# Optimization experiments

Measured on AMD Instinct MI355X. Metric: run time of the kernel, lower is better.

The kernel has to match this reference:

```python
import jax, jax.numpy as jnp
import numpy as np

N_NODES = 100000
N_EDGES = 1600000
NUM_FEATURES = 128
HIDDEN = 64
NUM_CLASSES = 2


def _gcn_norm(edge_index, num_nodes):
    # PyG gcn_norm: add self-loops, symmetric degree normalization.
    loop = jnp.arange(num_nodes, dtype=edge_index.dtype)
    src = jnp.concatenate([edge_index[0], loop])
    dst = jnp.concatenate([edge_index[1], loop])
    deg = jax.ops.segment_sum(jnp.ones_like(src, dtype=jnp.float32), dst,
                              num_segments=num_nodes)
    dinv = jnp.where(deg > 0, jax.lax.rsqrt(deg), 0.0)
    norm = dinv[src] * dinv[dst]  # [E + N]
    return src, dst, norm


def _gcn_conv(x, src, dst, norm, W, b, num_nodes):
    h = x @ W  # linear transform first (PyG GCNConv)
    msg = h[src] * norm[:, None]  # gather + edge scaling, [E+N, H]
    out = jax.ops.segment_sum(msg, dst, num_segments=num_nodes)  # scatter-add
    return out + b


def setup_inputs() -> dict:
    key = jax.random.key(0)
    ks = jax.random.split(key, 8)
    x = jax.random.normal(ks[0], (N_NODES, NUM_FEATURES), dtype=jnp.float32)
    edge_index = jax.random.randint(ks[1], (2, N_EDGES), 0, N_NODES, dtype=jnp.int32)
    def glorot(k, shape):
        lim = np.sqrt(6.0 / (shape[0] + shape[1]))
        return jax.random.uniform(k, shape, jnp.float32, -lim, lim)
    return {
        "x": x,
        "edge_index": edge_index,
        "W1": glorot(ks[2], (NUM_FEATURES, HIDDEN)),
        "b1": jnp.zeros((HIDDEN,), jnp.float32),
        "W2": glorot(ks[3], (HIDDEN, HIDDEN)),
        "b2": jnp.zeros((HIDDEN,), jnp.float32),
        "W3": glorot(ks[4], (HIDDEN, HIDDEN)),
        "b3": jnp.zeros((HIDDEN,), jnp.float32),
        "Wlin": glorot(ks[5], (HIDDEN, NUM_CLASSES)),
        "blin": jnp.zeros((NUM_CLASSES,), jnp.float32),
    }


def reference(x, edge_index, W1, b1, W2, b2, W3, b3, Wlin, blin):
    num_nodes = x.shape[0]
    src, dst, norm = _gcn_norm(edge_index, num_nodes)
    # eval mode: dropout is identity
    h = jax.nn.relu(_gcn_conv(x, src, dst, norm, W1, b1, num_nodes))
    h = jax.nn.relu(_gcn_conv(h, src, dst, norm, W2, b2, num_nodes))
    h = jax.nn.relu(_gcn_conv(h, src, dst, norm, W3, b3, num_nodes))
    logits = h @ Wlin + blin
    return jax.nn.log_softmax(logits, axis=1)
```

## Files before the change

kernel.cpp:

```cpp
#include <hip/hip_runtime.h>
#include <cstdint>
#include <cstddef>

#define NF 128
#define NH 64

typedef unsigned int uint32;
typedef short bf16x8 __attribute__((ext_vector_type(8)));
typedef float f32x4 __attribute__((ext_vector_type(4)));

__device__ inline unsigned short f2bf(float f) {
  unsigned int u = __float_as_uint(f);
  return (unsigned short)((u + 0x7FFF + ((u >> 16) & 1)) >> 16);
}
__device__ inline float bf2f_lo(uint32 u) { return __uint_as_float(u << 16); }
__device__ inline float bf2f_hi(uint32 u) { return __uint_as_float(u & 0xFFFF0000u); }


__global__ __launch_bounds__(256) void count_kernel(const int* __restrict__ ei, int E,
                                                    int* __restrict__ cnt, int RW) {
  int pass = blockIdx.x & 3;
  int i = (blockIdx.x >> 2) * 256 + threadIdx.x;
  if (i * 4 >= E) return;
  int4 d = ((const int4*)(ei + E))[i];
  int lo = pass * RW, hi = lo + RW;
  if (d.x >= lo && d.x < hi) atomicAdd(&cnt[d.x], 1);
  if (d.y >= lo && d.y < hi) atomicAdd(&cnt[d.y], 1);
  if (d.z >= lo && d.z < hi) atomicAdd(&cnt[d.z], 1);
  if (d.w >= lo && d.w < hi) atomicAdd(&cnt[d.w], 1);
}

__global__ __launch_bounds__(256) void partial_kernel(const int* __restrict__ cnt, int N,
                                                      int* __restrict__ part) {
  __shared__ int sd[256];
  int t = threadIdx.x;
  int idx = blockIdx.x * 1024 + t * 4;
  int s = 0;
#pragma unroll
  for (int j = 0; j < 4; ++j)
    if (idx + j < N) s += cnt[idx + j];
  sd[t] = s;
  __syncthreads();
  for (int off = 128; off > 0; off >>= 1) {
    if (t < off) sd[t] += sd[t + off];
    __syncthreads();
  }
  if (t == 0) part[blockIdx.x] = sd[0];
}

__global__ __launch_bounds__(128) void scanp_kernel(int* __restrict__ part, int NB,
                                                    int* __restrict__ rowptrN) {
  __shared__ int s[128];
  int t = threadIdx.x;
  int v = (t < NB) ? part[t] : 0;
  s[t] = v;
  __syncthreads();
  for (int off = 1; off < 128; off <<= 1) {
    int add = (t >= off) ? s[t - off] : 0;
    __syncthreads();
    s[t] += add;
    __syncthreads();
  }
  if (t < NB) part[t] = s[t] - v;
  if (t == 0) rowptrN[0] = s[127];
}

__global__ __launch_bounds__(256) void rowptr_kernel(const int* __restrict__ cnt,
                                                     const int* __restrict__ part,
                                                     int* __restrict__ rowptr,
                                                     int* __restrict__ cnt2,
                                                     float* __restrict__ dinv, int N) {
  __shared__ int s[256];
  int t = threadIdx.x;
  int idx = blockIdx.x * 1024 + t * 4;
  int c[4];
  int ts = 0;
#pragma unroll
  for (int j = 0; j < 4; ++j) {
    c[j] = (idx + j < N) ? cnt[idx + j] : 0;
    ts += c[j];
  }
  s[t] = ts;
  __syncthreads();
  for (int off = 1; off < 256; off <<= 1) {
    int add = (t >= off) ? s[t - off] : 0;
    __syncthreads();
    s[t] += add;
    __syncthreads();
  }
  int run = s[t] - ts + part[blockIdx.x];
#pragma unroll
  for (int j = 0; j < 4; ++j) {
    if (idx + j < N) {
      rowptr[idx + j] = run;
      cnt2[idx + j] = run;
      dinv[idx + j] = rsqrtf((float)(c[j] + 1));
    }
    run += c[j];
  }
}

__global__ __launch_bounds__(256) void fill_kernel(const int* __restrict__ ei, int E,
                                                   int* __restrict__ cnt2,
                                                   const float* __restrict__ dinv,
                                                   int2* __restrict__ col2, int RW) {
  int pass = blockIdx.x & 3;
  int i = (blockIdx.x >> 2) * 256 + threadIdx.x;
  if (i * 4 >= E) return;
  int4 sv = ((const int4*)ei)[i];
  int4 dv = ((const int4*)(ei + E))[i];
  int lo = pass * RW, hi = lo + RW;
  int ss[4] = {sv.x, sv.y, sv.z, sv.w};
  int dd[4] = {dv.x, dv.y, dv.z, dv.w};
#pragma unroll
  for (int j = 0; j < 4; ++j) {
    int d = dd[j];
    if (d < lo || d >= hi) continue;
    int s = ss[j];
    float w = dinv[s] * dinv[d];
    int pos = atomicAdd(&cnt2[d], 1);
    col2[pos] = make_int2(s, __float_as_int(w));
  }
}


__global__ __launch_bounds__(256) void gemm1_mfma_kernel(
    const float* __restrict__ X, const float* __restrict__ W,
    uint32* __restrict__ Hb, int N) {
  const int lane = threadIdx.x & 63;
  const int wv = threadIdx.x >> 6;
  const int m = lane & 15;
  const int g = lane >> 4;
  const int base = blockIdx.x * 64 + wv * 16;
  int row = base + m;
  int rowc = row < N ? row : N - 1;
  const float* xp = X + (size_t)rowc * 128 + g * 8;

  f32x4 acc[4];
#pragma unroll
  for (int nt = 0; nt < 4; ++nt) acc[nt] = (f32x4){0.f, 0.f, 0.f, 0.f};

#pragma unroll
  for (int kk = 0; kk < 4; ++kk) {
    float4 alo = *(const float4*)(xp + kk * 32);
    float4 ahi = *(const float4*)(xp + kk * 32 + 4);
    bf16x8 a;
    a[0] = (short)f2bf(alo.x); a[1] = (short)f2bf(alo.y);
    a[2] = (short)f2bf(alo.z); a[3] = (short)f2bf(alo.w);
    a[4] = (short)f2bf(ahi.x); a[5] = (short)f2bf(ahi.y);
    a[6] = (short)f2bf(ahi.z); a[7] = (short)f2bf(ahi.w);
    const float* wp = W + (size_t)(kk * 32 + g * 8) * 64 + m;
#pragma unroll
    for (int nt = 0; nt < 4; ++nt) {
      bf16x8 b;
#pragma unroll
      for (int i = 0; i < 8; ++i)
        b[i] = (short)f2bf(wp[(size_t)i * 64 + nt * 16]);
      acc[nt] = __builtin_amdgcn_mfma_f32_16x16x32_bf16(a, b, acc[nt], 0, 0, 0);
    }
  }
  unsigned short* Hs = (unsigned short*)Hb;
#pragma unroll
  for (int j = 0; j < 4; ++j) {
    int n = base + g * 4 + j;
    if (n < N) {
#pragma unroll
      for (int nt = 0; nt < 4; ++nt)
        Hs[(size_t)n * 64 + nt * 16 + m] = f2bf(acc[nt][j]);
    }
  }
}


template <int FINAL>
__global__ __launch_bounds__(256) void prop_fused_kernel(
    const uint32* __restrict__ H32, const int* __restrict__ rowptr,
    const int2* __restrict__ col2, const float* __restrict__ dinv,
    const float* __restrict__ bias, const float* __restrict__ Wn,
    const float* __restrict__ blin, void* __restrict__ outv, int N) {
  __shared__ float Ws[FINAL ? 4 : 64 * 64];
  __shared__ float rbuf[FINAL ? 1 : 4][64];
  const int lane = threadIdx.x & 63;
  const int widx = threadIdx.x >> 6;
  const int fl = lane & 31;
  const int half = lane >> 5;

  if (!FINAL) {
    const float4* Wg = (const float4*)Wn;
    float4* Wl = (float4*)Ws;
    for (int i = threadIdx.x; i < 1024; i += 256) Wl[i] = Wg[i];
    __syncthreads();
  }

  int n = blockIdx.x * 4 + widx;
  n = __builtin_amdgcn_readfirstlane(n);
  if (n >= N) return;

  int e0 = rowptr[n];
  int e1 = rowptr[n + 1];
  float di = dinv[n];
  const int2* ec = col2 + e0;
  const int m = e1 - e0;

  float acc0 = 0.f, acc1 = 0.f;
  if (half == 0) {
    uint32 u = H32[(size_t)n * 32 + fl];
    float w = di * di;
    acc0 = bf2f_lo(u) * w;
    acc1 = bf2f_hi(u) * w;
  }

  const int npair = m >> 1;
  const int nfull = npair >> 3;
  for (int b = 0; b < nfull; ++b) {
    int s[8];
    float wv[8];
#pragma unroll
    for (int j = 0; j < 8; ++j) {
      int2 c = ec[2 * (b * 8 + j) + half];
      s[j] = c.x;
      wv[j] = __int_as_float(c.y);
    }
    uint32 u[8];
#pragma unroll
    for (int j = 0; j < 8; ++j) u[j] = H32[(size_t)s[j] * 32 + fl];
#pragma unroll
    for (int j = 0; j < 8; ++j) {
      acc0 = fmaf(wv[j], bf2f_lo(u[j]), acc0);
      acc1 = fmaf(wv[j], bf2f_hi(u[j]), acc1);
    }
  }
  for (int t = nfull * 8; t < npair; ++t) {
    int2 c = ec[2 * t + half];
    uint32 u = H32[(size_t)c.x * 32 + fl];
    float w = __int_as_float(c.y);
    acc0 = fmaf(w, bf2f_lo(u), acc0);
    acc1 = fmaf(w, bf2f_hi(u), acc1);
  }
  if ((m & 1) && half == 0) {
    int2 c = ec[m - 1];
    uint32 u = H32[(size_t)c.x * 32 + fl];
    float w = __int_as_float(c.y);
    acc0 = fmaf(w, bf2f_lo(u), acc0);
    acc1 = fmaf(w, bf2f_hi(u), acc1);
  }
  acc0 += __shfl_xor(acc0, 32, 64);
  acc1 += __shfl_xor(acc1, 32, 64);

  float2 bv = ((const float2*)bias)[fl];
  float r0 = acc0 + bv.x;
  float r1 = acc1 + bv.y;
  r0 = r0 > 0.f ? r0 : 0.f;
  r1 = r1 > 0.f ? r1 : 0.f;

  if (FINAL) {
    float t0 = 0.f, t1 = 0.f;
    if (half == 0) {
      t0 = r0 * Wn[4 * fl + 0] + r1 * Wn[4 * fl + 2];
      t1 = r0 * Wn[4 * fl + 1] + r1 * Wn[4 * fl + 3];
    }
#pragma unroll
    for (int off = 32; off > 0; off >>= 1) {
      t0 += __shfl_xor(t0, off, 64);
      t1 += __shfl_xor(t1, off, 64);
    }
    if (lane == 0) {
      float* out = (float*)outv;
      float l0 = t0 + blin[0];
      float l1 = t1 + blin[1];
      float mx = fmaxf(l0, l1);
      float lz = mx + logf(expf(l0 - mx) + expf(l1 - mx));
      out[(size_t)n * 2 + 0] = l0 - lz;
      out[(size_t)n * 2 + 1] = l1 - lz;
    }
  } else {
    if (half == 0) *(float2*)(&rbuf[widx][2 * fl]) = make_float2(r0, r1);
    __builtin_amdgcn_wave_barrier();
    float o = 0.f;
#pragma unroll
    for (int q = 0; q < 16; ++q) {
      float4 rv = *(const float4*)(&rbuf[widx][4 * q]);
      o = fmaf(rv.x, Ws[(4 * q + 0) * 64 + lane], o);
      o = fmaf(rv.y, Ws[(4 * q + 1) * 64 + lane], o);
      o = fmaf(rv.z, Ws[(4 * q + 2) * 64 + lane], o);
      o = fmaf(rv.w, Ws[(4 * q + 3) * 64 + lane], o);
    }
    ((unsigned short*)outv)[(size_t)n * 64 + lane] = f2bf(o);
  }
}


extern "C" void kernel_launch(void* const* d_in, const int* in_sizes, int n_in,
                              void* d_out, int out_size, void* d_ws, size_t ws_size,
                              hipStream_t stream) {
  const float* x  = (const float*)d_in[0];
  const int*   ei = (const int*)d_in[1];
  const float* W1 = (const float*)d_in[2];
  const float* b1 = (const float*)d_in[3];
  const float* W2 = (const float*)d_in[4];
  const float* b2 = (const float*)d_in[5];
  const float* W3 = (const float*)d_in[6];
  const float* b3 = (const float*)d_in[7];
  const float* Wl = (const float*)d_in[8];
  const float* bl = (const float*)d_in[9];
  float* out = (float*)d_out;

  const int N = in_sizes[0] / NF;
  const int E = in_sizes[1] / 2;

  char* w = (char*)d_ws;
  size_t off = 0;
  auto alloc = [&](size_t bytes) {
    void* p = w + off;
    off += bytes;
    off = (off + 15) & ~(size_t)15;
    return p;
  };
  int*    cnt    = (int*)alloc((size_t)N * 4);
  int*    cnt2   = (int*)alloc((size_t)N * 4);
  int*    rowptr = (int*)alloc((size_t)(N + 1) * 4);
  int*    part   = (int*)alloc(256 * 4);
  float*  dinv   = (float*)alloc((size_t)N * 4);
  int2*   col2   = (int2*)alloc((size_t)E * 8);
  uint32* hA     = (uint32*)alloc((size_t)N * 32 * 4);
  uint32* hB     = (uint32*)alloc((size_t)N * 32 * 4);

  const int NB = (N + 1023) / 1024;
  const int RW4 = (N + 3) / 4;
  const int NCHUNK = (E / 4 + 255) / 256;

  hipMemsetAsync(cnt, 0, (size_t)N * 4, stream);
  hipLaunchKernelGGL(count_kernel, dim3(4 * NCHUNK), dim3(256), 0, stream,
                     ei, E, cnt, RW4);
  hipLaunchKernelGGL(partial_kernel, dim3(NB), dim3(256), 0, stream, cnt, N, part);
  hipLaunchKernelGGL(scanp_kernel, dim3(1), dim3(128), 0, stream, part, NB, rowptr + N);
  hipLaunchKernelGGL(rowptr_kernel, dim3(NB), dim3(256), 0, stream,
                     cnt, part, rowptr, cnt2, dinv, N);
  hipLaunchKernelGGL(fill_kernel, dim3(4 * NCHUNK), dim3(256), 0, stream,
                     ei, E, cnt2, dinv, col2, RW4);

  hipLaunchKernelGGL(gemm1_mfma_kernel, dim3((N + 63) / 64), dim3(256), 0, stream,
                     x, W1, hA, N);
  hipLaunchKernelGGL(prop_fused_kernel<0>, dim3((N + 3) / 4), dim3(256), 0, stream,
                     hA, rowptr, col2, dinv, b1, W2, (const float*)nullptr, (void*)hB, N);
  hipLaunchKernelGGL(prop_fused_kernel<0>, dim3((N + 3) / 4), dim3(256), 0, stream,
                     hB, rowptr, col2, dinv, b2, W3, (const float*)nullptr, (void*)hA, N);
  hipLaunchKernelGGL(prop_fused_kernel<1>, dim3((N + 3) / 4), dim3(256), 0, stream,
                     hA, rowptr, col2, dinv, b3, Wl, bl, (void*)out, N);
}
```

Measured before the change: 428.7 us.

## Fuse gemm1 with degree count; split layer-2 into sliced aggregation plus separate transform

Merges the first-layer MFMA GEMM and the edge degree-count into one launch, so the compute-bound GEMM blocks run alongside the atomic-bound counting blocks and one launch is removed. The second layer's fused aggregate-and-transform kernel is replaced by an aggregation kernel that splits the 64 features into two 32-wide slices across separate blocks, four edges per wave iteration, followed by a standalone tiled FP32 transform kernel. This aims to raise memory-level parallelism in the gather and move the dense transform out of the latency-bound gather kernel. In exchange it adds an extra bf16 write and read of the intermediate activations and reads the edge list twice.

After: 467.9 us. 9.1% more time.

```diff
diff --git a/kernel.cpp b/kernel.cpp
--- a/kernel.cpp
+++ b/kernel.cpp
@@ -17,17 +17,66 @@
 __device__ inline float bf2f_hi(uint32 u) { return __uint_as_float(u & 0xFFFF0000u); }
 
 
-__global__ __launch_bounds__(256) void count_kernel(const int* __restrict__ ei, int E,
-                                                    int* __restrict__ cnt, int RW) {
-  int pass = blockIdx.x & 3;
-  int i = (blockIdx.x >> 2) * 256 + threadIdx.x;
-  if (i * 4 >= E) return;
-  int4 d = ((const int4*)(ei + E))[i];
-  int lo = pass * RW, hi = lo + RW;
-  if (d.x >= lo && d.x < hi) atomicAdd(&cnt[d.x], 1);
-  if (d.y >= lo && d.y < hi) atomicAdd(&cnt[d.y], 1);
-  if (d.z >= lo && d.z < hi) atomicAdd(&cnt[d.z], 1);
-  if (d.w >= lo && d.w < hi) atomicAdd(&cnt[d.w], 1);
+__global__ __launch_bounds__(256) void gemm1_count_kernel(
+    const float* __restrict__ X, const float* __restrict__ W,
+    uint32* __restrict__ Hb, int N,
+    const int* __restrict__ ei, int E, int* __restrict__ cnt, int RW, int G1) {
+  if ((int)blockIdx.x >= G1) {
+    int b = blockIdx.x - G1;
+    int pass = b & 3;
+    int i = (b >> 2) * 256 + threadIdx.x;
+    if (i * 4 >= E) return;
+    int4 d = ((const int4*)(ei + E))[i];
+    int lo = pass * RW, hi = lo + RW;
+    if (d.x >= lo && d.x < hi) atomicAdd(&cnt[d.x], 1);
+    if (d.y >= lo && d.y < hi) atomicAdd(&cnt[d.y], 1);
+    if (d.z >= lo && d.z < hi) atomicAdd(&cnt[d.z], 1);
+    if (d.w >= lo && d.w < hi) atomicAdd(&cnt[d.w], 1);
+    return;
+  }
+
+  const int lane = threadIdx.x & 63;
+  const int wv = threadIdx.x >> 6;
+  const int m = lane & 15;
+  const int g = lane >> 4;
+  const int base = blockIdx.x * 64 + wv * 16;
+  int row = base + m;
+  int rowc = row < N ? row : N - 1;
+  const float* xp = X + (size_t)rowc * 128 + g * 8;
+
+  f32x4 acc[4];
+#pragma unroll
+  for (int nt = 0; nt < 4; ++nt) acc[nt] = (f32x4){0.f, 0.f, 0.f, 0.f};
+
+#pragma unroll
+  for (int kk = 0; kk < 4; ++kk) {
+    float4 alo = *(const float4*)(xp + kk * 32);
+    float4 ahi = *(const float4*)(xp + kk * 32 + 4);
+    bf16x8 a;
+    a[0] = (short)f2bf(alo.x); a[1] = (short)f2bf(alo.y);
+    a[2] = (short)f2bf(alo.z); a[3] = (short)f2bf(alo.w);
+    a[4] = (short)f2bf(ahi.x); a[5] = (short)f2bf(ahi.y);
+    a[6] = (short)f2bf(ahi.z); a[7] = (short)f2bf(ahi.w);
+    const float* wp = W + (size_t)(kk * 32 + g * 8) * 64 + m;
+#pragma unroll
+    for (int nt = 0; nt < 4; ++nt) {
+      bf16x8 b;
+#pragma unroll
+      for (int i = 0; i < 8; ++i)
+        b[i] = (short)f2bf(wp[(size_t)i * 64 + nt * 16]);
+      acc[nt] = __builtin_amdgcn_mfma_f32_16x16x32_bf16(a, b, acc[nt], 0, 0, 0);
+    }
+  }
+  unsigned short* Hs = (unsigned short*)Hb;
+#pragma unroll
+  for (int j = 0; j < 4; ++j) {
+    int n = base + g * 4 + j;
+    if (n < N) {
+#pragma unroll
+      for (int nt = 0; nt < 4; ++nt)
+        Hs[(size_t)n * 64 + nt * 16 + m] = f2bf(acc[nt][j]);
+    }
+  }
 }
 
 __global__ __launch_bounds__(256) void partial_kernel(const int* __restrict__ cnt, int N,
@@ -124,54 +173,6 @@
 }
 
 
-__global__ __launch_bounds__(256) void gemm1_mfma_kernel(
-    const float* __restrict__ X, const float* __restrict__ W,
-    uint32* __restrict__ Hb, int N) {
-  const int lane = threadIdx.x & 63;
-  const int wv = threadIdx.x >> 6;
-  const int m = lane & 15;
-  const int g = lane >> 4;
-  const int base = blockIdx.x * 64 + wv * 16;
-  int row = base + m;
-  int rowc = row < N ? row : N - 1;
-  const float* xp = X + (size_t)rowc * 128 + g * 8;
-
-  f32x4 acc[4];
-#pragma unroll
-  for (int nt = 0; nt < 4; ++nt) acc[nt] = (f32x4){0.f, 0.f, 0.f, 0.f};
-
-#pragma unroll
-  for (int kk = 0; kk < 4; ++kk) {
-    float4 alo = *(const float4*)(xp + kk * 32);
-    float4 ahi = *(const float4*)(xp + kk * 32 + 4);
-    bf16x8 a;
-    a[0] = (short)f2bf(alo.x); a[1] = (short)f2bf(alo.y);
-    a[2] = (short)f2bf(alo.z); a[3] = (short)f2bf(alo.w);
-    a[4] = (short)f2bf(ahi.x); a[5] = (short)f2bf(ahi.y);
-    a[6] = (short)f2bf(ahi.z); a[7] = (short)f2bf(ahi.w);
-    const float* wp = W + (size_t)(kk * 32 + g * 8) * 64 + m;
-#pragma unroll
-    for (int nt = 0; nt < 4; ++nt) {
-      bf16x8 b;
-#pragma unroll
-      for (int i = 0; i < 8; ++i)
-        b[i] = (short)f2bf(wp[(size_t)i * 64 + nt * 16]);
-      acc[nt] = __builtin_amdgcn_mfma_f32_16x16x32_bf16(a, b, acc[nt], 0, 0, 0);
-    }
-  }
-  unsigned short* Hs = (unsigned short*)Hb;
-#pragma unroll
-  for (int j = 0; j < 4; ++j) {
-    int n = base + g * 4 + j;
-    if (n < N) {
-#pragma unroll
-      for (int nt = 0; nt < 4; ++nt)
-        Hs[(size_t)n * 64 + nt * 16 + m] = f2bf(acc[nt][j]);
-    }
-  }
-}
-
-
 template <int FINAL>
 __global__ __launch_bounds__(256) void prop_fused_kernel(
     const uint32* __restrict__ H32, const int* __restrict__ rowptr,
@@ -286,6 +287,127 @@
       o = fmaf(rv.w, Ws[(4 * q + 3) * 64 + lane], o);
     }
     ((unsigned short*)outv)[(size_t)n * 64 + lane] = f2bf(o);
+  }
+}
+
+
+__global__ __launch_bounds__(256) void agg_half_kernel(
+    const uint32* __restrict__ H32, const int* __restrict__ rowptr,
+    const int2* __restrict__ col2, const float* __restrict__ dinv,
+    const float* __restrict__ bias, uint32* __restrict__ Rout, int N, int NBH) {
+  const int slice = (int)blockIdx.x >= NBH ? 1 : 0;
+  const int nb = blockIdx.x - slice * NBH;
+  const int lane = threadIdx.x & 63;
+  const int widx = threadIdx.x >> 6;
+  const int fl = lane & 15;
+  const int qtr = lane >> 4;
+
+  int n = nb * 4 + widx;
+  n = __builtin_amdgcn_readfirstlane(n);
+  if (n >= N) return;
+
+  int e0 = rowptr[n];
+  int m = rowptr[n + 1] - e0;
+  const int2* ec = col2 + e0;
+  float di = dinv[n];
+  const uint32* Hs = H32 + slice * 16 + fl;
+
+  float acc0 = 0.f, acc1 = 0.f;
+  const int nq = (m + 3) >> 2;
+  for (int it = 0; it < nq; ++it) {
+    int er = it * 4 + qtr;
+    bool v = er < m;
+    int2 c = ec[v ? er : 0];
+    float w = v ? __int_as_float(c.y) : 0.f;
+    uint32 u = Hs[(size_t)c.x * 32];
+    acc0 = fmaf(w, bf2f_lo(u), acc0);
+    acc1 = fmaf(w, bf2f_hi(u), acc1);
+  }
+  acc0 += __shfl_xor(acc0, 16, 64);
+  acc1 += __shfl_xor(acc1, 16, 64);
+  acc0 += __shfl_xor(acc0, 32, 64);
+  acc1 += __shfl_xor(acc1, 32, 64);
+
+  uint32 su = Hs[(size_t)n * 32];
+  float d2 = di * di;
+  acc0 = fmaf(d2, bf2f_lo(su), acc0);
+  acc1 = fmaf(d2, bf2f_hi(su), acc1);
+
+  float2 bv = ((const float2*)bias)[slice * 16 + fl];
+  float r0 = fmaxf(acc0 + bv.x, 0.f);
+  float r1 = fmaxf(acc1 + bv.y, 0.f);
+  if (qtr == 0) {
+    Rout[(size_t)n * 32 + slice * 16 + fl] =
+        (uint32)f2bf(r0) | ((uint32)f2bf(r1) << 16);
+  }
+}
+
+__global__ __launch_bounds__(256, 4) void transform_kernel(
+    const uint32* __restrict__ R, const float* __restrict__ W,
+    uint32* __restrict__ Hout, int N) {
+  __shared__ float XsT[64][68];
+  __shared__ float Ws[64 * 64];
+  const int tid = threadIdx.x;
+  const int n0 = blockIdx.x * 64;
+  const int tn = (tid >> 4) * 4;
+  const int tf = (tid & 15) * 4;
+  {
+    const float4* Wg = (const float4*)W;
+    float4* Wl = (float4*)Ws;
+#pragma unroll
+    for (int j = 0; j < 4; ++j) Wl[tid + j * 256] = Wg[tid + j * 256];
+  }
+#pragma unroll
+  for (int it = 0; it < 2; ++it) {
+    int sb = it * 256 + tid;
+    int n = sb >> 3;
+    int q = sb & 7;
+    uint4 v = make_uint4(0, 0, 0, 0);
+    if (n0 + n < N) v = *(const uint4*)(R + (size_t)(n0 + n) * 32 + q * 4);
+    XsT[q * 8 + 0][n] = bf2f_lo(v.x);
+    XsT[q * 8 + 1][n] = bf2f_hi(v.x);
+    XsT[q * 8 + 2][n] = bf2f_lo(v.y);
+    XsT[q * 8 + 3][n] = bf2f_hi(v.y);
+    XsT[q * 8 + 4][n] = bf2f_lo(v.z);
+    XsT[q * 8 + 5][n] = bf2f_hi(v.z);
+    XsT[q * 8 + 6][n] = bf2f_lo(v.w);
+    XsT[q * 8 + 7][n] = bf2f_hi(v.w);
+  }
+  __syncthreads();
+  float acc[4][4];
+#pragma unroll
+  for (int i = 0; i < 4; ++i)
+#pragma unroll
+    for (int j = 0; j < 4; ++j) acc[i][j] = 0.f;
+#pragma unroll 8
+  for (int k = 0; k < 64; ++k) {
+    float4 xv = *(const float4*)(&XsT[k][tn]);
+    float4 wv = *(const float4*)(&Ws[k * 64 + tf]);
+    acc[0][0] = fmaf(xv.x, wv.x, acc[0][0]);
+    acc[0][1] = fmaf(xv.x, wv.y, acc[0][1]);
+    acc[0][2] = fmaf(xv.x, wv.z, acc[0][2]);
+    acc[0][3] = fmaf(xv.x, wv.w, acc[0][3]);
+    acc[1][0] = fmaf(xv.y, wv.x, acc[1][0]);
+    acc[1][1] = fmaf(xv.y, wv.y, acc[1][1]);
+    acc[1][2] = fmaf(xv.y, wv.z, acc[1][2]);
+    acc[1][3] = fmaf(xv.y, wv.w, acc[1][3]);
+    acc[2][0] = fmaf(xv.z, wv.x, acc[2][0]);
+    acc[2][1] = fmaf(xv.z, wv.y, acc[2][1]);
+    acc[2][2] = fmaf(xv.z, wv.z, acc[2][2]);
+    acc[2][3] = fmaf(xv.z, wv.w, acc[2][3]);
+    acc[3][0] = fmaf(xv.w, wv.x, acc[3][0]);
+    acc[3][1] = fmaf(xv.w, wv.y, acc[3][1]);
+    acc[3][2] = fmaf(xv.w, wv.z, acc[3][2]);
+    acc[3][3] = fmaf(xv.w, wv.w, acc[3][3]);
+  }
+#pragma unroll
+  for (int i = 0; i < 4; ++i) {
+    int n = n0 + tn + i;
+    if (n < N) {
+      uint32 a = (uint32)f2bf(acc[i][0]) | ((uint32)f2bf(acc[i][1]) << 16);
+      uint32 b = (uint32)f2bf(acc[i][2]) | ((uint32)f2bf(acc[i][3]) << 16);
+      *(uint2*)(Hout + (size_t)n * 32 + tf / 2) = make_uint2(a, b);
+    }
   }
 }
 
@@ -328,10 +450,12 @@
   const int NB = (N + 1023) / 1024;
   const int RW4 = (N + 3) / 4;
   const int NCHUNK = (E / 4 + 255) / 256;
+  const int G1 = ((((N + 63) / 64) + 3) / 4) * 4;
+  const int NBH = (N + 3) / 4;
 
   hipMemsetAsync(cnt, 0, (size_t)N * 4, stream);
-  hipLaunchKernelGGL(count_kernel, dim3(4 * NCHUNK), dim3(256), 0, stream,
-                     ei, E, cnt, RW4);
+  hipLaunchKernelGGL(gemm1_count_kernel, dim3(G1 + 4 * NCHUNK), dim3(256), 0, stream,
+                     x, W1, hA, N, ei, E, cnt, RW4, G1);
   hipLaunchKernelGGL(partial_kernel, dim3(NB), dim3(256), 0, stream, cnt, N, part);
   hipLaunchKernelGGL(scanp_kernel, dim3(1), dim3(128), 0, stream, part, NB, rowptr + N);
   hipLaunchKernelGGL(rowptr_kernel, dim3(NB), dim3(256), 0, stream,
@@ -339,12 +463,12 @@
   hipLaunchKernelGGL(fill_kernel, dim3(4 * NCHUNK), dim3(256), 0, stream,
                      ei, E, cnt2, dinv, col2, RW4);
 
-  hipLaunchKernelGGL(gemm1_mfma_kernel, dim3((N + 63) / 64), dim3(256), 0, stream,
-                     x, W1, hA, N);
-  hipLaunchKernelGGL(prop_fused_kernel<0>, dim3((N + 3) / 4), dim3(256), 0, stream,
+  hipLaunchKernelGGL(prop_fused_kernel<0>, dim3(NBH), dim3(256), 0, stream,
                      hA, rowptr, col2, dinv, b1, W2, (const float*)nullptr, (void*)hB, N);
-  hipLaunchKernelGGL(prop_fused_kernel<0>, dim3((N + 3) / 4), dim3(256), 0, stream,
-                     hB, rowptr, col2, dinv, b2, W3, (const float*)nullptr, (void*)hA, N);
-  hipLaunchKernelGGL(prop_fused_kernel<1>, dim3((N + 3) / 4), dim3(256), 0, stream,
-                     hA, rowptr, col2, dinv, b3, Wl, bl, (void*)out, N);
-}
+  hipLaunchKernelGGL(agg_half_kernel, dim3(2 * NBH), dim3(256), 0, stream,
+                     hB, rowptr, col2, dinv, b2, hA, N, NBH);
+  hipLaunchKernelGGL(transform_kernel, dim3((N + 63) / 64), dim3(256), 0, stream,
+                     hA, W3, hB, N);
+  hipLaunchKernelGGL(prop_fused_kernel<1>, dim3(NBH), dim3(256), 0, stream,
+                     hB, rowptr, col2, dinv, b3, Wl, bl, (void*)out, N);
+}
```
